# Performance work log

Hardware: AMD Instinct MI355X
Metric: run time of the kernel (lower is better)

The kernel has to match this reference:

```python
import jax, jax.numpy as jnp
import numpy as np

N_NODES = 100000
N_EDGES = 3200000
N_GRAPHS = 512
IN_DIM, HID, OUT, N_CLS = 32, 64, 64, 10


def _linear_params(key, din, dout, scale=0.05):
    k1, k2 = jax.random.split(key)
    return (jax.random.normal(k1, (din, dout), jnp.float32) * scale,
            jax.random.normal(k2, (dout,), jnp.float32) * scale)


def setup_inputs() -> dict:
    key = jax.random.key(0)
    ks = jax.random.split(key, 12)
    x = jax.random.normal(ks[0], (N_NODES, IN_DIM), jnp.float32)
    edge_index = jax.random.randint(ks[1], (2, N_EDGES), 0, N_NODES, jnp.int64)
    batch = jnp.sort(jax.random.randint(ks[2], (N_NODES,), 0, N_GRAPHS, jnp.int64))
    W_emb, b_emb = _linear_params(ks[3], IN_DIM, HID)
    W1, b1 = _linear_params(ks[4], HID, HID)
    W2, b2 = _linear_params(ks[5], HID, HID)
    W3, b3 = _linear_params(ks[6], HID, HID)
    W4, b4 = _linear_params(ks[7], HID, OUT)
    Wr1, br1 = _linear_params(ks[8], OUT, OUT // 2)
    Wr2, br2 = _linear_params(ks[9], OUT // 2, OUT // 4)
    Wr3, br3 = _linear_params(ks[10], OUT // 4, N_CLS)
    return dict(x=x, edge_index=edge_index, batch=batch, n_graphs=N_GRAPHS,
                W_emb=W_emb, b_emb=b_emb, W1=W1, b1=b1, W2=W2, b2=b2,
                W3=W3, b3=b3, W4=W4, b4=b4, Wr1=Wr1, br1=br1,
                Wr2=Wr2, br2=br2, Wr3=Wr3, br3=br3)


def reference(x, edge_index, batch, n_graphs,
              W_emb, b_emb, W1, b1, W2, b2, W3, b3, W4, b4,
              Wr1, br1, Wr2, br2, Wr3, br3):
    n = x.shape[0]
    # PyG GCNConv(normalize=True): add self-loops, symmetric D^{-1/2} norm
    self_idx = jnp.arange(n, dtype=edge_index.dtype)
    src = jnp.concatenate([edge_index[0], self_idx])  # [E+N]
    dst = jnp.concatenate([edge_index[1], self_idx])
    deg = jax.ops.segment_sum(jnp.ones(src.shape[0], x.dtype), dst, num_segments=n)
    dis = jnp.where(deg > 0, jax.lax.rsqrt(deg), 0.0)
    norm = dis[src] * dis[dst]  # [E+N]

    def gcn_conv(h, W, b):
        h = h @ W                              # [N, D]
        msg = h[src] * norm[:, None]           # gather + scale, [E+N, D]
        agg = jax.ops.segment_sum(msg, dst, num_segments=n)  # scatter-add
        return agg + b

    h = x @ W_emb + b_emb
    h = jax.nn.relu(gcn_conv(h, W1, b1))
    h = jax.nn.relu(gcn_conv(h, W2, b2))
    h = jax.nn.relu(gcn_conv(h, W3, b3))
    h = jax.nn.relu(gcn_conv(h, W4, b4))

    # global mean pool over graphs
    sums = jax.ops.segment_sum(h, batch, num_segments=n_graphs)
    cnts = jax.ops.segment_sum(jnp.ones(n, h.dtype), batch, num_segments=n_graphs)
    pooled = sums / jnp.maximum(cnts, 1.0)[:, None]

    r = jax.nn.relu(pooled @ Wr1 + br1)
    r = jax.nn.relu(r @ Wr2 + br2)
    logits = r @ Wr3 + br3
    return jax.nn.log_softmax(logits, axis=1)
```

## Files before the change

kernel.cpp:

```cpp
#include <hip/hip_runtime.h>
#include <hip/hip_bf16.h>

typedef __hip_bfloat16 bf16;
typedef short bf16x8 __attribute__((ext_vector_type(8)));
typedef float f32x4 __attribute__((ext_vector_type(4)));
typedef float f32x2 __attribute__((ext_vector_type(2)));
typedef int i32x4 __attribute__((ext_vector_type(4)));
typedef unsigned u32x4 __attribute__((ext_vector_type(4)));

#define N_NODES 100000
#define N_EDGES 3200000
#define N_GRAPHS 512
#define NBKT    ((N_NODES + 255) / 256)
#define CAP     11776
#define EPB     16384
#define NBLK_A  ((N_EDGES + EPB - 1) / EPB)
#define FP4_SCALE 16.0f
#define FP4_INV   (1.0f / 16.0f)


__device__ inline void accf4(f32x2* ae, f32x2* ao, unsigned d) {
#if __has_builtin(__builtin_amdgcn_cvt_pk_f32_fp8) && __has_builtin(__builtin_amdgcn_perm)
    unsigned lo8 = __builtin_amdgcn_perm(0x4C484440u, 0x3C383000u, d & 0x07070707u)
                 | ((d & 0x08080808u) << 4);
    unsigned hi8 = __builtin_amdgcn_perm(0x4C484440u, 0x3C383000u, (d >> 4) & 0x07070707u)
                 | (d & 0x80808080u);
    ae[0] += __builtin_amdgcn_cvt_pk_f32_fp8((int)lo8, false);
    ae[1] += __builtin_amdgcn_cvt_pk_f32_fp8((int)lo8, true);
    ao[0] += __builtin_amdgcn_cvt_pk_f32_fp8((int)hi8, false);
    ao[1] += __builtin_amdgcn_cvt_pk_f32_fp8((int)hi8, true);
#else
    #pragma unroll
    for (int i = 0; i < 4; ++i) {
        unsigned by = (d >> (8 * i)) & 0xFFu;
        unsigned ln = by & 7u, hn = (by >> 4) & 7u;
        float lv = (ln < 2) ? (float)ln * 0.5f : 0.5f * (float)(1 << ((ln >> 1) - 1)) * (2 + (ln & 1));
        float hv = (hn < 2) ? (float)hn * 0.5f : 0.5f * (float)(1 << ((hn >> 1) - 1)) * (2 + (hn & 1));
        if (by & 8u) lv = -lv;
        if (by & 0x80u) hv = -hv;
        ae[i >> 1][i & 1] += lv;
        ao[i >> 1][i & 1] += hv;
    }
#endif
}


__device__ inline unsigned fp4n(float v) {
    unsigned s = (__float_as_uint(v) >> 28) & 8u;
    float x = fabsf(v);
    unsigned n = (unsigned)(x >= 0.25f) + (x >= 0.75f) + (x >= 1.25f) + (x >= 1.75f)
               + (x >= 2.5f) + (x >= 3.5f) + (x >= 5.0f);
    return s | n;
}

__device__ inline unsigned short f2bf(float x) {
    unsigned u = __float_as_uint(x);
    return (unsigned short)((u + 0x7FFF + ((u >> 16) & 1)) >> 16);
}


__global__ void k_setup(const float* __restrict__ W_emb, const float* __restrict__ b_emb,
                        const float* __restrict__ W1, const float* __restrict__ W2,
                        const float* __restrict__ W3, const float* __restrict__ W4,
                        float* __restrict__ Wc, float* __restrict__ bc,
                        unsigned short* __restrict__ Wfrag, int* __restrict__ gcur,
                        unsigned* __restrict__ ta, unsigned* __restrict__ tb) {
    int blk = blockIdx.x, t = threadIdx.x;
    if (blk == 0) {
        for (int i = t; i < 32 * 64; i += 256) {
            int a = i / 64, b = i % 64;
            float acc = 0.f;
            for (int k = 0; k < 64; ++k) acc += W_emb[a * 64 + k] * W1[k * 64 + b];
            Wc[i] = acc;
        }
        if (t < 64) {
            float acc = 0.f;
            for (int k = 0; k < 64; ++k) acc += b_emb[k] * W1[k * 64 + t];
            bc[t] = acc;
        }
    } else if (blk <= 3) {
        const float* W = (blk == 1) ? W2 : (blk == 2) ? W3 : W4;
        unsigned short* dst = Wfrag + (size_t)(blk - 1) * 4096;
        for (int i = 0; i < 16; ++i) {
            int flat = t * 16 + i;
            int j = flat & 7, lane = (flat >> 3) & 63, mt = (flat >> 9) & 3, kt = flat >> 11;
            int m = mt * 16 + (lane & 15);
            int k = kt * 32 + ((lane >> 4) << 3) + j;
            dst[flat] = f2bf(W[k * 64 + m]);
        }
    } else {
        for (int b = t; b < NBKT; b += 256) gcur[b] = b * CAP;
        if (t < 8) {
            size_t o = (size_t)N_NODES * 8 + t;
            ta[o] = 0; tb[o] = 0;
        }
    }
}


__global__ void __launch_bounds__(512) k_bucket(const int* __restrict__ ei,
                                                int* __restrict__ gcur,
                                                int* __restrict__ ebuf) {
    __shared__ int cnt[8][NBKT];
    __shared__ int base[8][NBKT];
    int t = threadIdx.x, w = t >> 6;
    for (int i = t; i < 8 * NBKT; i += 512) ((int*)cnt)[i] = 0;
    __syncthreads();
    int e0 = blockIdx.x * EPB + t;
    int sv[32], dv[32];
    #pragma unroll
    for (int j = 0; j < 32; ++j) {
        int e = e0 + j * 512;
        if (e < N_EDGES) {
            sv[j] = ei[e];
            dv[j] = ei[N_EDGES + e];
            atomicAdd(&cnt[w][dv[j] >> 8], 1);
        } else dv[j] = -1;
    }
    __syncthreads();
    for (int b = t; b < NBKT; b += 512) {
        int tot = 0, c[8];
        #pragma unroll
        for (int ww = 0; ww < 8; ++ww) { c[ww] = cnt[ww][b]; tot += c[ww]; }
        int g = tot ? atomicAdd(&gcur[b], tot) : 0;
        #pragma unroll
        for (int ww = 0; ww < 8; ++ww) { base[ww][b] = g; g += c[ww]; cnt[ww][b] = 0; }
    }
    __syncthreads();
    #pragma unroll
    for (int j = 0; j < 32; ++j) {
        if (dv[j] >= 0) {
            int b = dv[j] >> 8;
            int r = atomicAdd(&cnt[w][b], 1);
            ebuf[base[w][b] + r] = (sv[j] << 8) | (dv[j] & 255);
        }
    }
}


__global__ void __launch_bounds__(256) k_fill2(const int* __restrict__ ebuf,
                                               const int* __restrict__ gcur,
                                               int2* __restrict__ rc,
                                               float* __restrict__ dis,
                                               int* __restrict__ col) {
    __shared__ int cnt[256];
    __shared__ int sc[256];
    __shared__ int exs[256];
    __shared__ int cur[256];
    int b = blockIdx.x, t = threadIdx.x;
    int n0 = b * 256;
    int nrec = gcur[b] - b * CAP;
    const int* eb = ebuf + (size_t)b * CAP;
    int* cw = col + (size_t)b * CAP;
    cnt[t] = 0; cur[t] = 0;
    __syncthreads();
    for (int i = t; i < nrec; i += 256)
        atomicAdd(&cnt[eb[i] & 255], 1);
    __syncthreads();
    int c0 = cnt[t];
    int a16 = (c0 + 15) & ~15;
    sc[t] = a16; __syncthreads();
    for (int off = 1; off < 256; off <<= 1) {
        int u = (t >= off) ? sc[t - off] : 0;
        __syncthreads();
        sc[t] += u;
        __syncthreads();
    }
    int myex = sc[t] - a16;
    exs[t] = myex;
    int n = n0 + t;
    if (n < N_NODES) {
        rc[n] = make_int2(b * CAP + myex, c0);
        dis[n] = rsqrtf((float)(c0 + 1));
    }
    for (int i = myex + c0; i < myex + a16; ++i) cw[i] = N_NODES;
    __syncthreads();
    for (int i = t; i < nrec; i += 256) {
        int rec = eb[i];
        int dl = rec & 255;
        cw[exs[dl] + atomicAdd(&cur[dl], 1)] = rec >> 8;
    }
}


__global__ void __launch_bounds__(256) k_mm1(const float* __restrict__ inp,
                                             const float* __restrict__ W,
                                             const float* __restrict__ bias,
                                             const float* __restrict__ dis,
                                             unsigned char* __restrict__ T) {
    __shared__ float Wl[32][64];
    __shared__ float hs[16][32];
    int t = threadIdx.x;
    for (int i = t; i < 32 * 64; i += 256) Wl[i / 64][i % 64] = W[i];
    int row0 = blockIdx.x * 16;
    for (int i = t; i < 16 * 32; i += 256) {
        int r = row0 + i / 32, k = i % 32;
        hs[i / 32][k] = inp[(size_t)r * 32 + k];
    }
    __syncthreads();
    int c = t & 63, rg = t >> 6;
    float a0 = 0, a1 = 0, a2 = 0, a3 = 0;
    #pragma unroll 4
    for (int k = 0; k < 32; ++k) {
        float wv = Wl[k][c];
        a0 += hs[rg * 4 + 0][k] * wv;
        a1 += hs[rg * 4 + 1][k] * wv;
        a2 += hs[rg * 4 + 2][k] * wv;
        a3 += hs[rg * 4 + 3][k] * wv;
    }
    float bv = bias[c];
    int r = row0 + rg * 4;
    unsigned n0 = fp4n(FP4_SCALE * dis[r + 0] * (a0 + bv));
    unsigned n1 = fp4n(FP4_SCALE * dis[r + 1] * (a1 + bv));
    unsigned n2 = fp4n(FP4_SCALE * dis[r + 2] * (a2 + bv));
    unsigned n3 = fp4n(FP4_SCALE * dis[r + 3] * (a3 + bv));
    unsigned p0 = __shfl_xor(n0, 1), p1 = __shfl_xor(n1, 1);
    unsigned p2 = __shfl_xor(n2, 1), p3 = __shfl_xor(n3, 1);
    if ((c & 1) == 0) {
        size_t boff = (size_t)(c >> 1);
        T[(size_t)(r + 0) * 32 + boff] = (unsigned char)(n0 | (p0 << 4));
        T[(size_t)(r + 1) * 32 + boff] = (unsigned char)(n1 | (p1 << 4));
        T[(size_t)(r + 2) * 32 + boff] = (unsigned char)(n2 | (p2 << 4));
        T[(size_t)(r + 3) * 32 + boff] = (unsigned char)(n3 | (p3 << 4));
    }
}


template<bool LAST>
__global__ void __launch_bounds__(256, 8) k_aggc(const unsigned* __restrict__ tph,
                                                 const int2* __restrict__ rc,
                                                 const int* __restrict__ col,
                                                 const float* __restrict__ dis,
                                                 const float* __restrict__ bias,
                                                 const unsigned short* __restrict__ Wfrag,
                                                 unsigned char* __restrict__ Tn,
                                                 unsigned short* __restrict__ hout) {
    __shared__ unsigned short h_lds[32][72];
    int t = threadIdx.x;
    int rowbase = blockIdx.x * 32;
    int row = rowbase + (t >> 3);
    int sl = t & 7;
    f32x2 ae[2] = {{0.f, 0.f}, {0.f, 0.f}};
    f32x2 ao[2] = {{0.f, 0.f}, {0.f, 0.f}};
    accf4(ae, ao, tph[(size_t)row * 8 + sl]);
    int2 r = rc[row];
    int nit = (r.y + 15) >> 4;
    const int* cp = col + r.x;
    if (nit > 0) {
        i32x4 c0 = *(const i32x4*)(cp + 0);
        i32x4 c1 = *(const i32x4*)(cp + 4);
        i32x4 c2 = *(const i32x4*)(cp + 8);
        i32x4 c3 = *(const i32x4*)(cp + 12);
        for (int it = 1; ; ++it) {
            unsigned v0  = tph[(size_t)c0.x * 8 + sl];
            unsigned v1  = tph[(size_t)c0.y * 8 + sl];
            unsigned v2  = tph[(size_t)c0.z * 8 + sl];
            unsigned v3  = tph[(size_t)c0.w * 8 + sl];
            unsigned v4  = tph[(size_t)c1.x * 8 + sl];
            unsigned v5  = tph[(size_t)c1.y * 8 + sl];
            unsigned v6  = tph[(size_t)c1.z * 8 + sl];
            unsigned v7  = tph[(size_t)c1.w * 8 + sl];
            unsigned v8  = tph[(size_t)c2.x * 8 + sl];
            unsigned v9  = tph[(size_t)c2.y * 8 + sl];
            unsigned v10 = tph[(size_t)c2.z * 8 + sl];
            unsigned v11 = tph[(size_t)c2.w * 8 + sl];
            unsigned v12 = tph[(size_t)c3.x * 8 + sl];
            unsigned v13 = tph[(size_t)c3.y * 8 + sl];
            unsigned v14 = tph[(size_t)c3.z * 8 + sl];
            unsigned v15 = tph[(size_t)c3.w * 8 + sl];
            bool more = it < nit;
            if (more) {
                const int* np = cp + it * 16;
                c0 = *(const i32x4*)(np + 0);
                c1 = *(const i32x4*)(np + 4);
                c2 = *(const i32x4*)(np + 8);
                c3 = *(const i32x4*)(np + 12);
            }
            accf4(ae, ao, v0);  accf4(ae, ao, v1);  accf4(ae, ao, v2);  accf4(ae, ao, v3);
            accf4(ae, ao, v4);  accf4(ae, ao, v5);  accf4(ae, ao, v6);  accf4(ae, ao, v7);
            accf4(ae, ao, v8);  accf4(ae, ao, v9);  accf4(ae, ao, v10); accf4(ae, ao, v11);
            accf4(ae, ao, v12); accf4(ae, ao, v13); accf4(ae, ao, v14); accf4(ae, ao, v15);
            if (!more) break;
        }
    }
    float ds = dis[row] * FP4_INV;
    int f0 = sl * 8;
    float h0 = fmaxf(ds * ae[0].x + bias[f0 + 0], 0.f);
    float h1 = fmaxf(ds * ao[0].x + bias[f0 + 1], 0.f);
    float h2 = fmaxf(ds * ae[0].y + bias[f0 + 2], 0.f);
    float h3 = fmaxf(ds * ao[0].y + bias[f0 + 3], 0.f);
    float h4 = fmaxf(ds * ae[1].x + bias[f0 + 4], 0.f);
    float h5 = fmaxf(ds * ao[1].x + bias[f0 + 5], 0.f);
    float h6 = fmaxf(ds * ae[1].y + bias[f0 + 6], 0.f);
    float h7 = fmaxf(ds * ao[1].y + bias[f0 + 7], 0.f);
    u32x4 o;
    o.x = (unsigned)f2bf(h0) | ((unsigned)f2bf(h1) << 16);
    o.y = (unsigned)f2bf(h2) | ((unsigned)f2bf(h3) << 16);
    o.z = (unsigned)f2bf(h4) | ((unsigned)f2bf(h5) << 16);
    o.w = (unsigned)f2bf(h6) | ((unsigned)f2bf(h7) << 16);
    if (LAST) {
        *(u32x4*)(hout + (size_t)row * 64 + f0) = o;
        return;
    }
    *(u32x4*)&h_lds[row - rowbase][f0] = o;
    __syncthreads();
    int w = t >> 6, l = t & 63;
    int rg = w & 1, mt0 = (w >> 1) << 1;
    f32x4 acc[2] = {{0, 0, 0, 0}, {0, 0, 0, 0}};
    const bf16x8* wf = (const bf16x8*)Wfrag;
    #pragma unroll
    for (int kt = 0; kt < 2; ++kt) {
        bf16x8 bfr = *(const bf16x8*)&h_lds[rg * 16 + (l & 15)][kt * 32 + ((l >> 4) << 3)];
        #pragma unroll
        for (int mi = 0; mi < 2; ++mi) {
            bf16x8 afr = wf[(kt * 4 + mt0 + mi) * 64 + l];
            acc[mi] = __builtin_amdgcn_mfma_f32_16x16x32_bf16(afr, bfr, acc[mi], 0, 0, 0);
        }
    }
    int hrow = rowbase + rg * 16 + (l & 15);
    float sc2 = FP4_SCALE * dis[hrow];
    #pragma unroll
    for (int mi = 0; mi < 2; ++mi) {
        int colbase = (mt0 + mi) * 16 + ((l >> 4) << 2);
        unsigned short v = (unsigned short)(fp4n(sc2 * acc[mi][0])
                           | (fp4n(sc2 * acc[mi][1]) << 4)
                           | (fp4n(sc2 * acc[mi][2]) << 8)
                           | (fp4n(sc2 * acc[mi][3]) << 12));
        *(unsigned short*)(Tn + (size_t)hrow * 32 + (colbase >> 1)) = v;
    }
}


__global__ void __launch_bounds__(256) k_poolhead(const unsigned short* __restrict__ h,
                                                  const int* __restrict__ batch,
                                                  const float* __restrict__ Wr1, const float* __restrict__ br1,
                                                  const float* __restrict__ Wr2, const float* __restrict__ br2,
                                                  const float* __restrict__ Wr3, const float* __restrict__ br3,
                                                  float* __restrict__ out) {
    __shared__ float part[4][64];
    __shared__ float p[64], r1[32], r2[16], lg[10];
    __shared__ int seg[2];
    int g = blockIdx.x, t = threadIdx.x;
    if (t < 2) {
        int key = g + t;
        int lo = 0, hi = N_NODES;
        while (lo < hi) { int m = (lo + hi) >> 1; if (batch[m] < key) lo = m + 1; else hi = m; }
        seg[t] = lo;
    }
    __syncthreads();
    int start = seg[0], end = seg[1];
    int w = t >> 6, grp = (t >> 4) & 3, sl = t & 15;
    float a[4] = {0.f, 0.f, 0.f, 0.f};
    for (int r = start + w * 4 + grp; r < end; r += 16) {
        ushort4 v = *(const ushort4*)(h + (size_t)r * 64 + sl * 4);
        a[0] += __uint_as_float((unsigned)v.x << 16);
        a[1] += __uint_as_float((unsigned)v.y << 16);
        a[2] += __uint_as_float((unsigned)v.z << 16);
        a[3] += __uint_as_float((unsigned)v.w << 16);
    }
    #pragma unroll
    for (int j = 0; j < 4; ++j) {
        a[j] += __shfl_xor(a[j], 16);
        a[j] += __shfl_xor(a[j], 32);
    }
    if (sl == (t & 63)) {
        #pragma unroll
        for (int j = 0; j < 4; ++j) part[w][sl * 4 + j] = a[j];
    }
    __syncthreads();
    if (t < 64) {
        float s = part[0][t] + part[1][t] + part[2][t] + part[3][t];
        float c = fmaxf((float)(end - start), 1.f);
        p[t] = s / c;
    }
    __syncthreads();
    if (t < 32) {
        float acc = br1[t];
        for (int k = 0; k < 64; ++k) acc += p[k] * Wr1[k * 32 + t];
        r1[t] = fmaxf(acc, 0.f);
    }
    __syncthreads();
    if (t < 16) {
        float acc = br2[t];
        for (int k = 0; k < 32; ++k) acc += r1[k] * Wr2[k * 16 + t];
        r2[t] = fmaxf(acc, 0.f);
    }
    __syncthreads();
    if (t < 10) {
        float acc = br3[t];
        for (int k = 0; k < 16; ++k) acc += r2[k] * Wr3[k * 10 + t];
        lg[t] = acc;
    }
    __syncthreads();
    if (t < 10) {
        float m = -1e30f;
        for (int j = 0; j < 10; ++j) m = fmaxf(m, lg[j]);
        float s = 0.f;
        for (int j = 0; j < 10; ++j) s += expf(lg[j] - m);
        out[g * 10 + t] = lg[t] - m - logf(s);
    }
}

extern "C" void kernel_launch(void* const* d_in, const int* in_sizes, int n_in,
                              void* d_out, int out_size, void* d_ws, size_t ws_size,
                              hipStream_t stream) {
    const float* x     = (const float*)d_in[0];
    const int*   ei    = (const int*)d_in[1];
    const int*   batch = (const int*)d_in[2];
    const float* W_emb = (const float*)d_in[4];
    const float* b_emb = (const float*)d_in[5];
    const float* W1    = (const float*)d_in[6];
    const float* b1    = (const float*)d_in[7];
    const float* W2    = (const float*)d_in[8];
    const float* b2    = (const float*)d_in[9];
    const float* W3    = (const float*)d_in[10];
    const float* b3    = (const float*)d_in[11];
    const float* W4    = (const float*)d_in[12];
    const float* b4    = (const float*)d_in[13];
    const float* Wr1   = (const float*)d_in[14];
    const float* br1   = (const float*)d_in[15];
    const float* Wr2   = (const float*)d_in[16];
    const float* br2   = (const float*)d_in[17];
    const float* Wr3   = (const float*)d_in[18];
    const float* br3   = (const float*)d_in[19];
    float* out = (float*)d_out;

    char* ws = (char*)d_ws;
    size_t off = 0;
    auto alloc = [&](size_t b) { char* p = ws + off; off += (b + 511) & ~(size_t)511; return p; };
    size_t TBYTES = (size_t)(N_NODES + 1) * 32;
    int*   col    = (int*)  alloc((size_t)NBKT * CAP * 4);
    int*   ebuf   = (int*)  alloc((size_t)NBKT * CAP * 4);
    unsigned char* Ta = (unsigned char*)alloc(TBYTES);
    unsigned char* Tb = (unsigned char*)alloc(TBYTES);
    int2*  rc     = (int2*) alloc((size_t)N_NODES * 8);
    float* dis    = (float*)alloc((size_t)N_NODES * 4);
    int*   gcur   = (int*)  alloc((size_t)NBKT * 4);
    float* Wc     = (float*)alloc(32 * 64 * 4);
    float* bc     = (float*)alloc(64 * 4);
    unsigned short* Wfrag = (unsigned short*)alloc(3 * 4096 * 2);

    unsigned short* hout = (unsigned short*)ebuf;

    k_setup<<<5, 256, 0, stream>>>(W_emb, b_emb, W1, W2, W3, W4, Wc, bc, Wfrag, gcur,
                                   (unsigned*)Ta, (unsigned*)Tb);
    k_bucket<<<NBLK_A, 512, 0, stream>>>(ei, gcur, ebuf);
    k_fill2<<<NBKT, 256, 0, stream>>>(ebuf, gcur, rc, dis, col);

    int nbm = N_NODES / 16;
    int nba = N_NODES / 32;

    k_mm1<<<nbm, 256, 0, stream>>>(x, Wc, bc, dis, Ta);

    k_aggc<false><<<nba, 256, 0, stream>>>((const unsigned*)Ta, rc, col, dis, b1,
                                           Wfrag + 0 * 4096, Tb, nullptr);
    k_aggc<false><<<nba, 256, 0, stream>>>((const unsigned*)Tb, rc, col, dis, b2,
                                           Wfrag + 1 * 4096, Ta, nullptr);
    k_aggc<false><<<nba, 256, 0, stream>>>((const unsigned*)Ta, rc, col, dis, b3,
                                           Wfrag + 2 * 4096, Tb, nullptr);
    k_aggc<true><<<nba, 256, 0, stream>>>((const unsigned*)Tb, rc, col, dis, b4,
                                          nullptr, nullptr, hout);

    k_poolhead<<<N_GRAPHS, 256, 0, stream>>>(hout, batch, Wr1, br1, Wr2, br2, Wr3, br3, out);
}
```

Before: 234.4 us.

## Sort nodes by in-degree so aggregation blocks process similar-degree rows

Builds a degree histogram in k_fill2, then scans it and counting-sorts node ids by degree in two new kernels, producing a permutation. Each aggregation block now reads its row ids through that permutation, so threads in a wave handle rows with similar edge counts. This is meant to cut divergence and tail waiting inside waves during the gather loop. In exchange it adds two small kernel launches and an extra indirection, and output rows are now written to scattered locations instead of contiguous ones.

```diff
diff --git a/kernel.cpp b/kernel.cpp
--- a/kernel.cpp
+++ b/kernel.cpp
@@ -44,7 +44,6 @@
 #endif
 }
 
-
 __device__ inline unsigned fp4n(float v) {
     unsigned s = (__float_as_uint(v) >> 28) & 8u;
     float x = fabsf(v);
@@ -64,6 +63,7 @@
                         const float* __restrict__ W3, const float* __restrict__ W4,
                         float* __restrict__ Wc, float* __restrict__ bc,
                         unsigned short* __restrict__ Wfrag, int* __restrict__ gcur,
+                        int* __restrict__ dcnt,
                         unsigned* __restrict__ ta, unsigned* __restrict__ tb) {
     int blk = blockIdx.x, t = threadIdx.x;
     if (blk == 0) {
@@ -90,6 +90,7 @@
         }
     } else {
         for (int b = t; b < NBKT; b += 256) gcur[b] = b * CAP;
+        dcnt[t] = 0;
         if (t < 8) {
             size_t o = (size_t)N_NODES * 8 + t;
             ta[o] = 0; tb[o] = 0;
@@ -142,17 +143,19 @@
                                                const int* __restrict__ gcur,
                                                int2* __restrict__ rc,
                                                float* __restrict__ dis,
-                                               int* __restrict__ col) {
+                                               int* __restrict__ col,
+                                               int* __restrict__ dcnt) {
     __shared__ int cnt[256];
     __shared__ int sc[256];
     __shared__ int exs[256];
     __shared__ int cur[256];
+    __shared__ int dh[256];
     int b = blockIdx.x, t = threadIdx.x;
     int n0 = b * 256;
     int nrec = gcur[b] - b * CAP;
     const int* eb = ebuf + (size_t)b * CAP;
     int* cw = col + (size_t)b * CAP;
-    cnt[t] = 0; cur[t] = 0;
+    cnt[t] = 0; cur[t] = 0; dh[t] = 0;
     __syncthreads();
     for (int i = t; i < nrec; i += 256)
         atomicAdd(&cnt[eb[i] & 255], 1);
@@ -172,13 +175,52 @@
     if (n < N_NODES) {
         rc[n] = make_int2(b * CAP + myex, c0);
         dis[n] = rsqrtf((float)(c0 + 1));
+        atomicAdd(&dh[min(c0, 255)], 1);
     }
     for (int i = myex + c0; i < myex + a16; ++i) cw[i] = N_NODES;
     __syncthreads();
+    if (dh[t]) atomicAdd(&dcnt[t], dh[t]);
     for (int i = t; i < nrec; i += 256) {
         int rec = eb[i];
         int dl = rec & 255;
         cw[exs[dl] + atomicAdd(&cur[dl], 1)] = rec >> 8;
+    }
+}
+
+
+__global__ void k_dscan(const int* __restrict__ dcnt, int* __restrict__ dbase) {
+    __shared__ int lds[256];
+    int t = threadIdx.x;
+    int v = dcnt[t];
+    lds[t] = v; __syncthreads();
+    for (int off = 1; off < 256; off <<= 1) {
+        int u = (t >= off) ? lds[t - off] : 0;
+        __syncthreads();
+        lds[t] += u;
+        __syncthreads();
+    }
+    dbase[t] = lds[t] - v;
+}
+
+__global__ void __launch_bounds__(256) k_dsort(const int2* __restrict__ rc,
+                                               int* __restrict__ dbase,
+                                               int* __restrict__ perm) {
+    __shared__ int cnt[256];
+    __shared__ int base[256];
+    int b = blockIdx.x, t = threadIdx.x;
+    int n = b * 256 + t;
+    int bin = -1;
+    if (n < N_NODES) bin = min(rc[n].y, 255);
+    cnt[t] = 0;
+    __syncthreads();
+    if (bin >= 0) atomicAdd(&cnt[bin], 1);
+    __syncthreads();
+    if (cnt[t]) base[t] = atomicAdd(&dbase[t], cnt[t]);
+    cnt[t] = 0;
+    __syncthreads();
+    if (bin >= 0) {
+        int r = atomicAdd(&cnt[bin], 1);
+        perm[base[bin] + r] = n;
     }
 }
 
@@ -230,6 +272,7 @@
 __global__ void __launch_bounds__(256, 8) k_aggc(const unsigned* __restrict__ tph,
                                                  const int2* __restrict__ rc,
                                                  const int* __restrict__ col,
+                                                 const int* __restrict__ perm,
                                                  const float* __restrict__ dis,
                                                  const float* __restrict__ bias,
                                                  const unsigned short* __restrict__ Wfrag,
@@ -238,7 +281,8 @@
     __shared__ unsigned short h_lds[32][72];
     int t = threadIdx.x;
     int rowbase = blockIdx.x * 32;
-    int row = rowbase + (t >> 3);
+    int li = t >> 3;
+    int row = perm[rowbase + li];
     int sl = t & 7;
     f32x2 ae[2] = {{0.f, 0.f}, {0.f, 0.f}};
     f32x2 ao[2] = {{0.f, 0.f}, {0.f, 0.f}};
@@ -302,7 +346,7 @@
         *(u32x4*)(hout + (size_t)row * 64 + f0) = o;
         return;
     }
-    *(u32x4*)&h_lds[row - rowbase][f0] = o;
+    *(u32x4*)&h_lds[li][f0] = o;
     __syncthreads();
     int w = t >> 6, l = t & 63;
     int rg = w & 1, mt0 = (w >> 1) << 1;
@@ -317,7 +361,7 @@
             acc[mi] = __builtin_amdgcn_mfma_f32_16x16x32_bf16(afr, bfr, acc[mi], 0, 0, 0);
         }
     }
-    int hrow = rowbase + rg * 16 + (l & 15);
+    int hrow = perm[rowbase + rg * 16 + (l & 15)];
     float sc2 = FP4_SCALE * dis[hrow];
     #pragma unroll
     for (int mi = 0; mi < 2; ++mi) {
@@ -435,7 +479,10 @@
     unsigned char* Tb = (unsigned char*)alloc(TBYTES);
     int2*  rc     = (int2*) alloc((size_t)N_NODES * 8);
     float* dis    = (float*)alloc((size_t)N_NODES * 4);
+    int*   perm   = (int*)  alloc((size_t)(NBKT * 256) * 4);
     int*   gcur   = (int*)  alloc((size_t)NBKT * 4);
+    int*   dcnt   = (int*)  alloc(256 * 4);
+    int*   dbase  = (int*)  alloc(256 * 4);
     float* Wc     = (float*)alloc(32 * 64 * 4);
     float* bc     = (float*)alloc(64 * 4);
     unsigned short* Wfrag = (unsigned short*)alloc(3 * 4096 * 2);
@@ -443,22 +490,24 @@
     unsigned short* hout = (unsigned short*)ebuf;
 
     k_setup<<<5, 256, 0, stream>>>(W_emb, b_emb, W1, W2, W3, W4, Wc, bc, Wfrag, gcur,
-                                   (unsigned*)Ta, (unsigned*)Tb);
+                                   dcnt, (unsigned*)Ta, (unsigned*)Tb);
     k_bucket<<<NBLK_A, 512, 0, stream>>>(ei, gcur, ebuf);
-    k_fill2<<<NBKT, 256, 0, stream>>>(ebuf, gcur, rc, dis, col);
+    k_fill2<<<NBKT, 256, 0, stream>>>(ebuf, gcur, rc, dis, col, dcnt);
+    k_dscan<<<1, 256, 0, stream>>>(dcnt, dbase);
+    k_dsort<<<NBKT, 256, 0, stream>>>(rc, dbase, perm);
 
     int nbm = N_NODES / 16;
-    int nba = N_NODES / 32;
+    int nba = (N_NODES + 31) / 32;
 
     k_mm1<<<nbm, 256, 0, stream>>>(x, Wc, bc, dis, Ta);
 
-    k_aggc<false><<<nba, 256, 0, stream>>>((const unsigned*)Ta, rc, col, dis, b1,
+    k_aggc<false><<<nba, 256, 0, stream>>>((const unsigned*)Ta, rc, col, perm, dis, b1,
                                            Wfrag + 0 * 4096, Tb, nullptr);
-    k_aggc<false><<<nba, 256, 0, stream>>>((const unsigned*)Tb, rc, col, dis, b2,
+    k_aggc<false><<<nba, 256, 0, stream>>>((const unsigned*)Tb, rc, col, perm, dis, b2,
                                            Wfrag + 1 * 4096, Ta, nullptr);
-    k_aggc<false><<<nba, 256, 0, stream>>>((const unsigned*)Ta, rc, col, dis, b3,
+    k_aggc<false><<<nba, 256, 0, stream>>>((const unsigned*)Ta, rc, col, perm, dis, b3,
                                            Wfrag + 2 * 4096, Tb, nullptr);
-    k_aggc<true><<<nba, 256, 0, stream>>>((const unsigned*)Tb, rc, col, dis, b4,
+    k_aggc<true><<<nba, 256, 0, stream>>>((const unsigned*)Tb, rc, col, perm, dis, b4,
                                           nullptr, nullptr, hout);
 
     k_poolhead<<<N_GRAPHS, 256, 0, stream>>>(hout, batch, Wr1, br1, Wr2, br2, Wr3, br3, out);
```

New measurement: 241.3 us. 2.9% more time.
